# Optimization experiments

Measured on AMD Instinct MI355X. Metric: run time of the kernel, lower is better.

## Reference

```python
import jax, jax.numpy as jnp
import numpy as np

B, K = 262144, 128

def setup_inputs() -> dict:
    key = jax.random.key(0)
    k1, k2, k3 = jax.random.split(key, 3)
    logits = jax.random.normal(k1, (B, K), dtype=jnp.float32)
    labels = jax.random.randint(k2, (B,), 0, K, dtype=jnp.int32)
    # guarantee every bin's risk set {j: labels_j >= k} is non-empty
    labels = labels.at[0].set(K - 1)
    events = jax.random.randint(k3, (B,), 0, 2, dtype=jnp.int32)
    return {"logits": logits, "labels": labels, "events": events}

def reference(logits, labels, events):
    Bn, Kn = logits.shape
    ev = (events == 1)
    evf = ev.astype(logits.dtype)
    # logits at each sample's own bin: f(x_i, t_{label_i})
    own = jnp.take_along_axis(logits, labels[:, None], axis=1)[:, 0]  # (B,)
    # per-bin event counts and numerators via scatter-add (segment sum)
    n_ev = jnp.zeros((Kn,), logits.dtype).at[labels].add(evf)          # (K,)
    numer = jnp.zeros((Kn,), logits.dtype).at[labels].add(evf * own)   # (K,)
    # risk set R_k = {j : labels_j >= k}; masked per-column logsumexp
    risk_mask = labels[:, None] >= jnp.arange(Kn, dtype=labels.dtype)[None, :]  # (B,K)
    masked = jnp.where(risk_mask, logits, -jnp.inf)
    denom_log = jax.nn.logsumexp(masked, axis=0)                       # (K,)
    terms = jnp.where(n_ev > 0, numer - n_ev * denom_log, jnp.zeros((), logits.dtype))
    n_events_total = jnp.maximum(evf.sum(), jnp.ones((), logits.dtype))
    return -terms.sum() / n_events_total
```

## Files before the change

kernel.cpp:

```cpp
#include <hip/hip_runtime.h>
#include <math.h>

#define KBINS 128
#define NTHR  256

__global__ __launch_bounds__(NTHR) void cox_main(
    const float* __restrict__ logits, const int* __restrict__ labels,
    const int* __restrict__ events, float* __restrict__ part_denom,
    int* __restrict__ part_hist, float* __restrict__ part_s1,
    int* __restrict__ part_ev, int B)
{
    __shared__ float partLds[4][KBINS];
    __shared__ int   hist[KBINS];
    __shared__ float s1w[4];
    __shared__ int   evw[4];

    const int t    = threadIdx.x;
    const int wave = t >> 6;
    const int lane = t & 63;
    if (t < KBINS) hist[t] = 0;
    __syncthreads();

    const int c0 = lane << 1;
    float sa = 0.f, sb = 0.f;
    float accOwn = 0.f;
    int   accEv  = 0;

    const int stride = gridDim.x * 4;
    for (int r = blockIdx.x * 4 + wave; r < B; r += stride) {
        const float2 v = *reinterpret_cast<const float2*>(
            logits + (size_t)r * KBINS + c0);
        const int lab = labels[r];
        const int ev  = events[r];
        const float e0 = __expf(v.x);
        const float e1 = __expf(v.y);
        if (lab >= c0) sa += e0;
        if (lab >  c0) sb += e1;
        if ((lab >> 1) == lane) {
            if (ev) {
                accOwn += (lab & 1) ? v.y : v.x;
                atomicAdd(&hist[lab], 1);
            }
        }
        if (lane == 0) accEv += ev;
    }

    for (int off = 32; off; off >>= 1) {
        accOwn += __shfl_down(accOwn, off);
    }
    if (lane == 0) { s1w[wave] = accOwn; evw[wave] = accEv; }
    partLds[wave][c0]     = sa;
    partLds[wave][c0 + 1] = sb;
    __syncthreads();

    if (t < KBINS) {
        const int o = blockIdx.x * KBINS + t;
        part_denom[o] = partLds[0][t] + partLds[1][t] + partLds[2][t] + partLds[3][t];
        part_hist[o]  = hist[t];
    }
    if (t == 0) {
        part_s1[blockIdx.x] = s1w[0] + s1w[1] + s1w[2] + s1w[3];
        part_ev[blockIdx.x] = evw[0] + evw[1] + evw[2] + evw[3];
    }
}

__global__ __launch_bounds__(256) void cox_fin1(
    const float* __restrict__ part_denom, const int* __restrict__ part_hist,
    double* __restrict__ term, int nblk)
{
    const int k = blockIdx.x;
    const int t = threadIdx.x;
    double d = 0.0;
    int    h = 0;
    for (int b = t; b < nblk; b += 256) {
        d += (double)part_denom[(size_t)b * KBINS + k];
        h += part_hist[(size_t)b * KBINS + k];
    }
    __shared__ double ds[256];
    __shared__ int    hs[256];
    ds[t] = d; hs[t] = h;
    __syncthreads();
    for (int off = 128; off; off >>= 1) {
        if (t < off) { ds[t] += ds[t + off]; hs[t] += hs[t + off]; }
        __syncthreads();
    }
    if (t == 0) term[k] = (hs[0] > 0) ? (double)hs[0] * log(ds[0]) : 0.0;
}

__global__ __launch_bounds__(256) void cox_fin2(
    const double* __restrict__ term, const float* __restrict__ part_s1,
    const int* __restrict__ part_ev, float* __restrict__ out, int nblk)
{
    const int t = threadIdx.x;
    double s2 = (t < KBINS) ? term[t] : 0.0;
    double s1 = 0.0;
    int    ne = 0;
    for (int b = t; b < nblk; b += 256) {
        s1 += (double)part_s1[b];
        ne += part_ev[b];
    }
    __shared__ double a[256];
    __shared__ double c[256];
    __shared__ int    e[256];
    a[t] = s2; c[t] = s1; e[t] = ne;
    __syncthreads();
    for (int off = 128; off; off >>= 1) {
        if (t < off) { a[t] += a[t + off]; c[t] += c[t + off]; e[t] += e[t + off]; }
        __syncthreads();
    }
    if (t == 0) {
        double ntot = (double)(e[0] > 1 ? e[0] : 1);
        out[0] = (float)((a[0] - c[0]) / ntot);
    }
}

extern "C" void kernel_launch(void* const* d_in, const int* in_sizes, int n_in,
                              void* d_out, int out_size, void* d_ws, size_t ws_size,
                              hipStream_t stream) {
    const float* logits = (const float*)d_in[0];
    const int*   labels = (const int*)d_in[1];
    const int*   events = (const int*)d_in[2];
    const int B = in_sizes[1];

    int nblk = 2048;
    auto need = [](size_t nb) {
        return nb * KBINS * 4
             + nb * KBINS * 4
             + nb * 4
             + nb * 4
             + KBINS * 8 + 64;
    };
    while (nblk > 64 && need((size_t)nblk) > ws_size) nblk >>= 1;

    char* ws = (char*)d_ws;
    float*  part_denom = (float*)ws;
    int*    part_hist  = (int*)(ws + (size_t)nblk * KBINS * 4);
    float*  part_s1    = (float*)(ws + (size_t)2 * nblk * KBINS * 4);
    int*    part_ev    = (int*)(ws + (size_t)2 * nblk * KBINS * 4 + (size_t)nblk * 4);
    double* term       = (double*)(ws + (size_t)2 * nblk * KBINS * 4 + (size_t)2 * nblk * 4);

    cox_main<<<nblk, NTHR, 0, stream>>>(logits, labels, events,
                                        part_denom, part_hist, part_s1, part_ev, B);
    cox_fin1<<<KBINS, 256, 0, stream>>>(part_denom, part_hist, term, nblk);
    cox_fin2<<<1, 256, 0, stream>>>(term, part_s1, part_ev, (float*)d_out, nblk);
}
```

Measured before the change: 199.3 us.

## Use float4 half-wave rows, register histograms, and transposed partials for reduction

The main kernel now assigns one row per half-wave and loads float4 per lane, so each block covers 8 rows per iteration. Per-bin event counts move from LDS atomics into per-thread registers. Partials are written bin-major so the first finalize kernel reads them contiguously. The s1 and event-count reductions move into an extra fin1 block, which shrinks fin2 to a single-wave-pair shuffle reduction; in exchange the main loop does more compare and branch work per element.

Measured after the change: 201.6 us. Within noise of the previous version (+1.2%).

```diff
diff --git a/kernel.cpp b/kernel.cpp
--- a/kernel.cpp
+++ b/kernel.cpp
@@ -8,109 +8,125 @@
     const float* __restrict__ logits, const int* __restrict__ labels,
     const int* __restrict__ events, float* __restrict__ part_denom,
     int* __restrict__ part_hist, float* __restrict__ part_s1,
-    int* __restrict__ part_ev, int B)
+    int* __restrict__ part_ev, int B, int nblk)
 {
-    __shared__ float partLds[4][KBINS];
-    __shared__ int   hist[KBINS];
-    __shared__ float s1w[4];
-    __shared__ int   evw[4];
+    __shared__ float dsum[8][KBINS];
+    __shared__ int   hsum[8][KBINS];
+    __shared__ float s1sh[8];
+    __shared__ int   evsh[8];
 
     const int t    = threadIdx.x;
     const int wave = t >> 6;
     const int lane = t & 63;
-    if (t < KBINS) hist[t] = 0;
-    __syncthreads();
+    const int half = lane >> 5;
+    const int l32  = lane & 31;
+    const int hid  = wave * 2 + half;
+    const int c0   = l32 << 2;
 
-    const int c0 = lane << 1;
-    float sa = 0.f, sb = 0.f;
+    float sa0 = 0.f, sa1 = 0.f, sa2 = 0.f, sa3 = 0.f;
+    int   h0 = 0, h1 = 0, h2 = 0, h3 = 0;
     float accOwn = 0.f;
     int   accEv  = 0;
 
-    const int stride = gridDim.x * 4;
-    for (int r = blockIdx.x * 4 + wave; r < B; r += stride) {
-        const float2 v = *reinterpret_cast<const float2*>(
-            logits + (size_t)r * KBINS + c0);
-        const int lab = labels[r];
-        const int ev  = events[r];
+    const float4* __restrict__ lg4 = reinterpret_cast<const float4*>(logits);
+    const int rowsPerIter = nblk * 8;
+
+    #pragma unroll 2
+    for (int r = blockIdx.x * 8 + hid; r < B; r += rowsPerIter) {
+        const float4 v  = lg4[(size_t)r * (KBINS / 4) + l32];
+        const int   lab = labels[r];
+        const int   ev  = events[r];
         const float e0 = __expf(v.x);
         const float e1 = __expf(v.y);
-        if (lab >= c0) sa += e0;
-        if (lab >  c0) sb += e1;
-        if ((lab >> 1) == lane) {
-            if (ev) {
-                accOwn += (lab & 1) ? v.y : v.x;
-                atomicAdd(&hist[lab], 1);
-            }
+        const float e2 = __expf(v.z);
+        const float e3 = __expf(v.w);
+        if (lab >= c0    ) sa0 += e0;
+        if (lab >= c0 + 1) sa1 += e1;
+        if (lab >= c0 + 2) sa2 += e2;
+        if (lab >= c0 + 3) sa3 += e3;
+        if (ev) {
+            if      (lab == c0    ) { accOwn += v.x; h0++; }
+            else if (lab == c0 + 1) { accOwn += v.y; h1++; }
+            else if (lab == c0 + 2) { accOwn += v.z; h2++; }
+            else if (lab == c0 + 3) { accOwn += v.w; h3++; }
+            if (l32 == 0) accEv++;
         }
-        if (lane == 0) accEv += ev;
     }
 
-    for (int off = 32; off; off >>= 1) {
-        accOwn += __shfl_down(accOwn, off);
-    }
-    if (lane == 0) { s1w[wave] = accOwn; evw[wave] = accEv; }
-    partLds[wave][c0]     = sa;
-    partLds[wave][c0 + 1] = sb;
+    dsum[hid][c0    ] = sa0;  hsum[hid][c0    ] = h0;
+    dsum[hid][c0 + 1] = sa1;  hsum[hid][c0 + 1] = h1;
+    dsum[hid][c0 + 2] = sa2;  hsum[hid][c0 + 2] = h2;
+    dsum[hid][c0 + 3] = sa3;  hsum[hid][c0 + 3] = h3;
+
+    for (int off = 16; off; off >>= 1)
+        accOwn += __shfl_down(accOwn, off, 32);
+    if (l32 == 0) { s1sh[hid] = accOwn; evsh[hid] = accEv; }
     __syncthreads();
 
     if (t < KBINS) {
-        const int o = blockIdx.x * KBINS + t;
-        part_denom[o] = partLds[0][t] + partLds[1][t] + partLds[2][t] + partLds[3][t];
-        part_hist[o]  = hist[t];
+        float d = 0.f; int h = 0;
+        #pragma unroll
+        for (int i = 0; i < 8; ++i) { d += dsum[i][t]; h += hsum[i][t]; }
+        const size_t o = (size_t)t * nblk + blockIdx.x;
+        part_denom[o] = d;
+        part_hist[o]  = h;
     }
     if (t == 0) {
-        part_s1[blockIdx.x] = s1w[0] + s1w[1] + s1w[2] + s1w[3];
-        part_ev[blockIdx.x] = evw[0] + evw[1] + evw[2] + evw[3];
+        float s1 = 0.f; int e = 0;
+        #pragma unroll
+        for (int i = 0; i < 8; ++i) { s1 += s1sh[i]; e += evsh[i]; }
+        part_s1[blockIdx.x] = s1;
+        part_ev[blockIdx.x] = e;
     }
 }
 
 __global__ __launch_bounds__(256) void cox_fin1(
     const float* __restrict__ part_denom, const int* __restrict__ part_hist,
+    const float* __restrict__ part_s1, const int* __restrict__ part_ev,
     double* __restrict__ term, int nblk)
 {
     const int k = blockIdx.x;
     const int t = threadIdx.x;
+    __shared__ double ds[256];
+    __shared__ long   hs[256];
+
     double d = 0.0;
-    int    h = 0;
-    for (int b = t; b < nblk; b += 256) {
-        d += (double)part_denom[(size_t)b * KBINS + k];
-        h += part_hist[(size_t)b * KBINS + k];
+    long   h = 0;
+    if (k < KBINS) {
+        const float* pd = part_denom + (size_t)k * nblk;
+        const int*   ph = part_hist  + (size_t)k * nblk;
+        for (int b = t; b < nblk; b += 256) { d += (double)pd[b]; h += ph[b]; }
+    } else {
+        for (int b = t; b < nblk; b += 256) { d += (double)part_s1[b]; h += part_ev[b]; }
     }
-    __shared__ double ds[256];
-    __shared__ int    hs[256];
     ds[t] = d; hs[t] = h;
     __syncthreads();
     for (int off = 128; off; off >>= 1) {
         if (t < off) { ds[t] += ds[t + off]; hs[t] += hs[t + off]; }
         __syncthreads();
     }
-    if (t == 0) term[k] = (hs[0] > 0) ? (double)hs[0] * log(ds[0]) : 0.0;
+    if (t == 0) {
+        if (k < KBINS) term[k] = (hs[0] > 0) ? (double)hs[0] * log(ds[0]) : 0.0;
+        else { term[KBINS] = ds[0]; term[KBINS + 1] = (double)hs[0]; }
+    }
 }
 
-__global__ __launch_bounds__(256) void cox_fin2(
-    const double* __restrict__ term, const float* __restrict__ part_s1,
-    const int* __restrict__ part_ev, float* __restrict__ out, int nblk)
+__global__ __launch_bounds__(128) void cox_fin2(
+    const double* __restrict__ term, float* __restrict__ out)
 {
     const int t = threadIdx.x;
-    double s2 = (t < KBINS) ? term[t] : 0.0;
-    double s1 = 0.0;
-    int    ne = 0;
-    for (int b = t; b < nblk; b += 256) {
-        s1 += (double)part_s1[b];
-        ne += part_ev[b];
-    }
-    __shared__ double a[256];
-    __shared__ double c[256];
-    __shared__ int    e[256];
-    a[t] = s2; c[t] = s1; e[t] = ne;
+    double v = term[t];
+    for (int off = 32; off; off >>= 1)
+        v += __shfl_down(v, off, 64);
+    __shared__ double w[2];
+    if ((t & 63) == 0) w[t >> 6] = v;
     __syncthreads();
-    for (int off = 128; off; off >>= 1) {
-        if (t < off) { a[t] += a[t + off]; c[t] += c[t + off]; e[t] += e[t + off]; }
-        __syncthreads();
-    }
     if (t == 0) {
-        double ntot = (double)(e[0] > 1 ? e[0] : 1);
-        out[0] = (float)((a[0] - c[0]) / ntot);
+        const double s2   = w[0] + w[1];
+        const double s1   = term[KBINS];
+        const double ne   = term[KBINS + 1];
+        const double ntot = ne > 1.0 ? ne : 1.0;
+        out[0] = (float)((s2 - s1) / ntot);
     }
 }
 
@@ -124,11 +140,9 @@
 
     int nblk = 2048;
     auto need = [](size_t nb) {
-        return nb * KBINS * 4
-             + nb * KBINS * 4
-             + nb * 4
-             + nb * 4
-             + KBINS * 8 + 64;
+        return nb * KBINS * 4 * 2
+             + nb * 8
+             + (KBINS + 2) * 8 + 64;
     };
     while (nblk > 64 && need((size_t)nblk) > ws_size) nblk >>= 1;
 
@@ -140,7 +154,9 @@
     double* term       = (double*)(ws + (size_t)2 * nblk * KBINS * 4 + (size_t)2 * nblk * 4);
 
     cox_main<<<nblk, NTHR, 0, stream>>>(logits, labels, events,
-                                        part_denom, part_hist, part_s1, part_ev, B);
-    cox_fin1<<<KBINS, 256, 0, stream>>>(part_denom, part_hist, term, nblk);
-    cox_fin2<<<1, 256, 0, stream>>>(term, part_s1, part_ev, (float*)d_out, nblk);
+                                        part_denom, part_hist, part_s1, part_ev,
+                                        B, nblk);
+    cox_fin1<<<KBINS + 1, 256, 0, stream>>>(part_denom, part_hist,
+                                            part_s1, part_ev, term, nblk);
+    cox_fin2<<<1, 128, 0, stream>>>(term, (float*)d_out);
 }
```
